# Optimization experiments

Measured on AMD Instinct MI355X. Metric: run time of the kernel, lower is better.

## Reference

```python
import jax, jax.numpy as jnp
import numpy as np


def setup_inputs() -> dict:
    key = jax.random.key(0)
    k1, k2, k3, k4 = jax.random.split(key, 4)
    N, Ck, Cv, T, H, W = 8, 128, 512, 8, 30, 30
    return {
        "q_key": jax.random.normal(k1, (N, Ck, H, W), dtype=jnp.float32),
        "q_val": jax.random.normal(k2, (N, Cv, H, W), dtype=jnp.float32),
        "m_key": jax.random.normal(k3, (N, Ck, T, H, W), dtype=jnp.float32),
        "m_val": jax.random.normal(k4, (N, Cv, T, H, W), dtype=jnp.float32),
    }


def reference(q_key, q_val, m_key, m_val):
    N, Ck, H, W = q_key.shape
    _, Cv, T, Hm, Wm = m_val.shape
    qk = q_key.reshape(N, Ck, H * W)            # n c q
    mk = m_key.reshape(N, Ck, T * Hm * Wm)      # n c m
    # affinity [n, q, m], scaled by 1/sqrt(Ck)
    aff = jnp.einsum("ncq,ncm->nqm", qk, mk) * (Ck ** -0.5)
    # NOTE: softmax over the QUERY axis (axis=1), per the original module
    attn = jax.nn.softmax(aff, axis=1)
    mv = m_val.reshape(N, Cv, T * Hm * Wm)      # n c m
    mapped = jnp.einsum("nqm,ncm->ncq", attn, mv).reshape(N, Cv, Hm, Wm)
    return jnp.concatenate([q_val, mapped], axis=1)  # [N, 2*Cv, H, W]
```

## Files before the change

kernel.cpp:

```cpp
#include <hip/hip_runtime.h>
#include <stdint.h>

#define N_  8
#define CK  128
#define CV  512
#define HW  900
#define M_  7200
#define QK_SCALE 0.08838834764831845f

typedef __attribute__((ext_vector_type(8))) short  short8;
typedef __attribute__((ext_vector_type(4))) float  floatx4;
typedef __attribute__((ext_vector_type(4))) unsigned int   uintx4;
typedef __attribute__((ext_vector_type(4))) unsigned short ushortx4;

__device__ __forceinline__ uint16_t f32_to_bf16(float x) {
    union { float f; uint32_t u; } v; v.f = x;
    return (uint16_t)((v.u + 0x7FFFu + ((v.u >> 16) & 1u)) >> 16);
}

__device__ __forceinline__ void gload_lds16(const uint16_t* g, short* l) {
    __builtin_amdgcn_global_load_lds(
        (const __attribute__((address_space(1))) void*)g,
        (__attribute__((address_space(3))) void*)l,
        16, 0, 0);
}

#define WAITV(n) asm volatile("s_waitcnt vmcnt(" #n ")" ::: "memory")
#define BARRIER() do { __builtin_amdgcn_sched_barrier(0); \
                       __builtin_amdgcn_s_barrier(); \
                       __builtin_amdgcn_sched_barrier(0); } while (0)

__global__ void k_zero(float* __restrict__ p) {
    int i = blockIdx.x * 256 + threadIdx.x;
    if (i < N_ * M_) p[i] = 0.f;
}

__global__ __launch_bounds__(256) void k_copy_qval(const float* __restrict__ qv,
                                                   float* __restrict__ out) {
    unsigned i = blockIdx.x * 256 + threadIdx.x;
    unsigned e = i * 4u;
    unsigned n = e / (CV * HW);
    unsigned off = e - n * (CV * HW);
    *(floatx4*)&out[(size_t)n * (2 * CV * HW) + off] = *(const floatx4*)&qv[e];
}

__global__ __launch_bounds__(256) void k_trans(const float* __restrict__ in,
                                               uint16_t* __restrict__ outp, int L) {
    __shared__ float tile[32][33];
    const int tx = threadIdx.x & 31;
    const int ty = threadIdx.x >> 5;
    const int l0 = blockIdx.x * 32;
    const int c0 = blockIdx.y * 32;
    const int n  = blockIdx.z;
    const float* src = in + (size_t)n * CK * L;
    uint16_t* dst = outp + (size_t)n * L * CK;
#pragma unroll
    for (int p = 0; p < 4; p++) {
        int c = c0 + p * 8 + ty;
        int l = l0 + tx;
        float v = 0.f;
        if (l < L) v = src[(size_t)c * L + l];
        tile[p * 8 + ty][tx] = v;
    }
    __syncthreads();
#pragma unroll
    for (int p = 0; p < 4; p++) {
        int l = l0 + p * 8 + ty;
        int c = c0 + tx;
        if (l < L) dst[(size_t)l * CK + c] = f32_to_bf16(tile[tx][p * 8 + ty]);
    }
}

#define K1_TS 144

__global__ __launch_bounds__(256) void k1_gemm_exp(
    const uint16_t* __restrict__ qkT,
    const uint16_t* __restrict__ mkT,
    uint16_t* __restrict__ E,
    float* __restrict__ dsum)
{
    __shared__ __align__(16) short smem[32768];
    __shared__ float colsum[128];

    const int bid = blockIdx.x + 57 * (blockIdx.y + 8 * blockIdx.z);
    const int swz = (bid & 7) * 456 + (bid >> 3);
    const int mb   = swz % 57;
    const int rest = swz / 57;
    const int m0 = mb * 128;
    const int q0 = (rest & 7) * 128;
    const int n  = rest >> 3;
    const int tid = threadIdx.x;

    if (tid < 128) colsum[tid] = 0.f;

    const int lane = tid & 63;
    const int wid  = tid >> 6;
    const int wq   = (wid >> 1) << 6;
    const int wm   = (wid & 1) << 6;
    const int fr   = lane & 15;
    const int quad = lane >> 4;

    const int ca = wid * 2;
    const int rr = lane >> 2;
    const int cc = (lane & 3) * 8;

    const uint16_t* Ab = qkT + (size_t)n * HW * CK;
    const uint16_t* Bb = mkT + (size_t)n * M_ * CK;
    const uint16_t* A0p = Ab + (size_t)(q0 + ca * 16 + rr) * CK + cc;
    const uint16_t* A1p = A0p + 16 * CK;
    const uint16_t* B0p = Bb + (size_t)(m0 + ca * 16 + rr) * CK + cc;
    const uint16_t* B1p = B0p + 16 * CK;

    floatx4 acc[4][4];
#pragma unroll
    for (int a = 0; a < 4; a++)
#pragma unroll
        for (int b = 0; b < 4; b++) acc[a][b] = (floatx4){0.f, 0.f, 0.f, 0.f};

#define K1_STAGE(buf, ko) do { \
    short* dA = smem + (buf) * 8192 + ca * 512; \
    short* dB = dA + 4096; \
    gload_lds16(A0p + (ko), dA); \
    gload_lds16(A1p + (ko), dA + 512); \
    gload_lds16(B0p + (ko), dB); \
    gload_lds16(B1p + (ko), dB + 512); \
} while (0)

#define K1_COMPUTE(buf) do { \
    const short* bA = smem + (buf) * 8192; \
    const short* bB = bA + 4096; \
    const int k0 = quad * 8; \
    short8 af[4], bfr[4]; \
    _Pragma("unroll") \
    for (int t = 0; t < 4; t++) \
        af[t] = *(const short8*)&bA[(wq + t * 16 + fr) * 32 + k0]; \
    _Pragma("unroll") \
    for (int t = 0; t < 4; t++) \
        bfr[t] = *(const short8*)&bB[(wm + t * 16 + fr) * 32 + k0]; \
    _Pragma("unroll") \
    for (int tq = 0; tq < 4; tq++) \
        _Pragma("unroll") \
        for (int tm = 0; tm < 4; tm++) \
            acc[tq][tm] = __builtin_amdgcn_mfma_f32_16x16x32_bf16( \
                af[tq], bfr[tm], acc[tq][tm], 0, 0, 0); \
} while (0)

    K1_STAGE(0, 0); K1_STAGE(1, 32); K1_STAGE(2, 64);
    WAITV(8); BARRIER(); K1_STAGE(3, 96); K1_COMPUTE(0);
    WAITV(8); BARRIER(); K1_COMPUTE(1);
    WAITV(4); BARRIER(); K1_COMPUTE(2);
    WAITV(0); BARRIER(); K1_COMPUTE(3);

    __syncthreads();
    float cs[4] = {0.f, 0.f, 0.f, 0.f};
#pragma unroll
    for (int tq = 0; tq < 4; tq++) {
#pragma unroll
        for (int tm = 0; tm < 4; tm++) {
            const int col = wm + tm * 16 + fr;
#pragma unroll
            for (int i = 0; i < 4; i++) {
                const int row = wq + tq * 16 + quad * 4 + i;
                float e = __expf(acc[tq][tm][i] * QK_SCALE);
                if (q0 + row < HW) cs[tm] += e;
                smem[row * K1_TS + col] = (short)f32_to_bf16(e);
            }
        }
    }
#pragma unroll
    for (int tm = 0; tm < 4; tm++) {
        float s = cs[tm];
        s += __shfl_xor(s, 16, 64);
        s += __shfl_xor(s, 32, 64);
        if (quad == 0) atomicAdd(&colsum[wm + tm * 16 + fr], s);
    }
    __syncthreads();

    uint16_t* En = E + (size_t)n * HW * M_;
#pragma unroll
    for (int j = 0; j < 8; j++) {
        int idx = tid + j * 256;
        int r   = idx >> 4;
        int c8  = (idx & 15) * 8;
        if (q0 + r < HW && m0 + c8 + 8 <= M_) {
            uintx4 v = *(const uintx4*)&smem[r * K1_TS + c8];
            *(uintx4*)&En[(size_t)(q0 + r) * M_ + m0 + c8] = v;
        }
    }
    if (tid < 128) {
        const int gm = m0 + tid;
        if (gm < M_) atomicAdd(&dsum[(size_t)n * M_ + gm], colsum[tid]);
    }
#undef K1_STAGE
#undef K1_COMPUTE
}

__global__ void k_dinv(const float* __restrict__ d, float* __restrict__ di) {
    int i = blockIdx.x * 256 + threadIdx.x;
    if (i < N_ * M_) di[i] = 1.0f / d[i];
}

__global__ __launch_bounds__(256) void k_mvs(
    const float* __restrict__ mval,
    const float* __restrict__ dinv,
    uint16_t* __restrict__ mvs)
{
    unsigned i = blockIdx.x * 256 + threadIdx.x;
    unsigned base = i * 4u;
    unsigned n = base / (unsigned)(CV * M_);
    unsigned m = base % (unsigned)M_;
    floatx4 v  = *(const floatx4*)&mval[base];
    floatx4 di = *(const floatx4*)&dinv[n * (unsigned)M_ + m];
    ushortx4 o;
    o[0] = f32_to_bf16(v[0] * di[0]);
    o[1] = f32_to_bf16(v[1] * di[1]);
    o[2] = f32_to_bf16(v[2] * di[2]);
    o[3] = f32_to_bf16(v[3] * di[3]);
    *(ushortx4*)&mvs[base] = o;
}

#define K2_SPLITS 3
#define K2_BK 32
#define K2_STEPS 75

__global__ __launch_bounds__(256) void k2_split3(
    const uint16_t* __restrict__ mvs,
    const uint16_t* __restrict__ E,
    float* __restrict__ partials)
{
    __shared__ __align__(16) short lds2[32768];

    const int bid = blockIdx.x + 8 * (blockIdx.y + 4 * blockIdx.z);
    const int swz = (bid & 7) * 96 + (bid >> 3);
    const int q0 = (swz & 7) << 7;
    const int c0 = ((swz >> 3) & 3) << 7;
    const int nz = swz >> 5;
    const int n     = nz / K2_SPLITS;
    const int split = nz - n * K2_SPLITS;
    const int tid = threadIdx.x;

    const int lane = tid & 63;
    const int wid  = tid >> 6;
    const int wc   = (wid >> 1) << 6;
    const int wq   = (wid & 1) << 6;
    const int fr   = lane & 15;
    const int quad = lane >> 4;

    const int ca = wid * 2;
    const int rr = lane >> 2;
    const int cc = (lane & 3) * 8;

    const uint16_t* Asrc = mvs + (size_t)(n * CV + c0) * M_ + split * 2400;
    const uint16_t* Bsrc = E + (size_t)n * HW * M_ + split * 2400;
    const uint16_t* A0p = Asrc + (size_t)(ca * 16 + rr) * M_ + cc;
    const uint16_t* A1p = A0p + (size_t)16 * M_;
    const uint16_t* B0p = Bsrc + (size_t)(q0 + ca * 16 + rr) * M_ + cc;
    const uint16_t* B1p = B0p + (size_t)16 * M_;

    floatx4 acc[4][4];
#pragma unroll
    for (int a = 0; a < 4; a++)
#pragma unroll
        for (int b = 0; b < 4; b++) acc[a][b] = (floatx4){0.f, 0.f, 0.f, 0.f};

#define K2_STAGE(buf, mo) do { \
    short* dA = lds2 + (buf) * 8192 + ca * 512; \
    short* dB = dA + 4096; \
    gload_lds16(A0p + (mo), dA); \
    gload_lds16(A1p + (mo), dA + 512); \
    gload_lds16(B0p + (mo), dB); \
    gload_lds16(B1p + (mo), dB + 512); \
} while (0)

#define K2_COMPUTE(buf) do { \
    const short* bA = lds2 + (buf) * 8192; \
    const short* bB = bA + 4096; \
    const int k0 = quad * 8; \
    short8 af[4], bfr[4]; \
    _Pragma("unroll") \
    for (int t = 0; t < 4; t++) \
        af[t] = *(const short8*)&bA[(wc + t * 16 + fr) * 32 + k0]; \
    _Pragma("unroll") \
    for (int t = 0; t < 4; t++) \
        bfr[t] = *(const short8*)&bB[(wq + t * 16 + fr) * 32 + k0]; \
    _Pragma("unroll") \
    for (int tc = 0; tc < 4; tc++) \
        _Pragma("unroll") \
        for (int tq = 0; tq < 4; tq++) \
            acc[tc][tq] = __builtin_amdgcn_mfma_f32_16x16x32_bf16( \
                af[tc], bfr[tq], acc[tc][tq], 0, 0, 0); \
} while (0)

    K2_STAGE(0, 0);
    K2_STAGE(1, K2_BK);
    K2_STAGE(2, 2 * K2_BK);
    for (int t = 0; t < K2_STEPS - 3; ++t) {
        WAITV(8); BARRIER();
        K2_STAGE((t + 3) & 3, (t + 3) * K2_BK);
        K2_COMPUTE(t & 3);
    }
    WAITV(8); BARRIER(); K2_COMPUTE(0);
    WAITV(4); BARRIER(); K2_COMPUTE(1);
    WAITV(0); BARRIER(); K2_COMPUTE(2);

    float* P = partials + ((size_t)split * N_ + n) * CV * HW;
#pragma unroll
    for (int tc = 0; tc < 4; tc++) {
#pragma unroll
        for (int tq = 0; tq < 4; tq++) {
            const int gq = q0 + wq + tq * 16 + fr;
            if (gq < HW) {
#pragma unroll
                for (int i = 0; i < 4; i++) {
                    const int gc = c0 + wc + tc * 16 + quad * 4 + i;
                    P[(size_t)gc * HW + gq] = acc[tc][tq][i];
                }
            }
        }
    }
#undef K2_STAGE
#undef K2_COMPUTE
}

__global__ __launch_bounds__(256) void k_reduce3(const float* __restrict__ partials,
                                                 float* __restrict__ out) {
    unsigned i = blockIdx.x * 256 + threadIdx.x;
    unsigned e = i * 4u;
    unsigned n = e / (CV * HW);
    unsigned off = e - n * (CV * HW);
    const size_t stride = (size_t)N_ * CV * HW;
    const float* p = partials + (size_t)n * CV * HW + off;
    floatx4 a = *(const floatx4*)&p[0];
    floatx4 b = *(const floatx4*)&p[stride];
    floatx4 c = *(const floatx4*)&p[2 * stride];
    floatx4 s = a + b + c;
    *(floatx4*)&out[(size_t)n * (2 * CV * HW) + CV * HW + off] = s;
}

extern "C" void kernel_launch(void* const* d_in, const int* in_sizes, int n_in,
                              void* d_out, int out_size, void* d_ws, size_t ws_size,
                              hipStream_t stream) {
    const float* qkey = (const float*)d_in[0];
    const float* qval = (const float*)d_in[1];
    const float* mkey = (const float*)d_in[2];
    const float* mval = (const float*)d_in[3];
    float* out = (float*)d_out;

    char* ws = (char*)d_ws;
    uint16_t* E        = (uint16_t*)ws;
    float*    dsum     = (float*)(ws + 103680000);
    float*    dinv     = (float*)(ws + 103910400);
    uint16_t* mvs      = (uint16_t*)(ws + 104140800);
    float*    partials = (float*)(ws + 163123200);
    uint16_t* qkT      = (uint16_t*)(ws + 163123200);
    uint16_t* mkT      = (uint16_t*)(ws + 163123200 + 1843200);

    (void)in_sizes; (void)n_in; (void)out_size; (void)ws_size;

    k_zero<<<dim3((N_ * M_ + 255) / 256), 256, 0, stream>>>(dsum);
    k_copy_qval<<<dim3((N_ * CV * HW) / 4 / 256), 256, 0, stream>>>(qval, out);
    k_trans<<<dim3(29, 4, N_), 256, 0, stream>>>(qkey, qkT, HW);
    k_trans<<<dim3(225, 4, N_), 256, 0, stream>>>(mkey, mkT, M_);
    k1_gemm_exp<<<dim3(57, 8, N_), 256, 0, stream>>>(qkT, mkT, E, dsum);
    k_dinv<<<dim3((N_ * M_ + 255) / 256), 256, 0, stream>>>(dsum, dinv);
    k_mvs<<<dim3((N_ * CV * M_) / 4 / 256), 256, 0, stream>>>(mval, dinv, mvs);
    k2_split3<<<dim3(8, 4, N_ * K2_SPLITS), 256, 0, stream>>>(mvs, E, partials);
    k_reduce3<<<dim3((N_ * CV * HW) / 4 / 256), 256, 0, stream>>>(partials, out);
}
```

Baseline: 414.8 us.

## Remove split-K in second GEMM, load E directly to registers, fuse reciprocal

Drops the three-way split-K and the reduction kernel, so the second GEMM writes final output directly. The E operand is loaded straight from global memory into registers with a 3-stage rotating buffer, while only mvs is staged in LDS. The reciprocal of the column sums is folded into the mvs scaling kernel, removing a launch. This removes the partials traffic and two launches, but cuts the grid to 256 blocks with long K loops and uses less coalesced direct global loads.

```diff
diff --git a/kernel.cpp b/kernel.cpp
--- a/kernel.cpp
+++ b/kernel.cpp
@@ -195,50 +195,41 @@
 #undef K1_COMPUTE
 }
 
-__global__ void k_dinv(const float* __restrict__ d, float* __restrict__ di) {
-    int i = blockIdx.x * 256 + threadIdx.x;
-    if (i < N_ * M_) di[i] = 1.0f / d[i];
-}
-
 __global__ __launch_bounds__(256) void k_mvs(
     const float* __restrict__ mval,
-    const float* __restrict__ dinv,
+    const float* __restrict__ dsum,
     uint16_t* __restrict__ mvs)
 {
     unsigned i = blockIdx.x * 256 + threadIdx.x;
     unsigned base = i * 4u;
     unsigned n = base / (unsigned)(CV * M_);
     unsigned m = base % (unsigned)M_;
-    floatx4 v  = *(const floatx4*)&mval[base];
-    floatx4 di = *(const floatx4*)&dinv[n * (unsigned)M_ + m];
+    floatx4 v = *(const floatx4*)&mval[base];
+    floatx4 d = *(const floatx4*)&dsum[n * (unsigned)M_ + m];
     ushortx4 o;
-    o[0] = f32_to_bf16(v[0] * di[0]);
-    o[1] = f32_to_bf16(v[1] * di[1]);
-    o[2] = f32_to_bf16(v[2] * di[2]);
-    o[3] = f32_to_bf16(v[3] * di[3]);
+    o[0] = f32_to_bf16(v[0] * (1.0f / d[0]));
+    o[1] = f32_to_bf16(v[1] * (1.0f / d[1]));
+    o[2] = f32_to_bf16(v[2] * (1.0f / d[2]));
+    o[3] = f32_to_bf16(v[3] * (1.0f / d[3]));
     *(ushortx4*)&mvs[base] = o;
 }
 
-#define K2_SPLITS 3
-#define K2_BK 32
-#define K2_STEPS 75
-
-__global__ __launch_bounds__(256) void k2_split3(
+#define K2_NT 225
+
+__global__ __launch_bounds__(256) void k2_direct(
     const uint16_t* __restrict__ mvs,
     const uint16_t* __restrict__ E,
-    float* __restrict__ partials)
+    float* __restrict__ out)
 {
-    __shared__ __align__(16) short lds2[32768];
+    __shared__ __align__(16) short ldsA[3 * 4096];
 
     const int bid = blockIdx.x + 8 * (blockIdx.y + 4 * blockIdx.z);
-    const int swz = (bid & 7) * 96 + (bid >> 3);
+    const int swz = (bid & 7) * 32 + (bid >> 3);
     const int q0 = (swz & 7) << 7;
     const int c0 = ((swz >> 3) & 3) << 7;
-    const int nz = swz >> 5;
-    const int n     = nz / K2_SPLITS;
-    const int split = nz - n * K2_SPLITS;
-    const int tid = threadIdx.x;
-
+    const int n  = swz >> 5;
+
+    const int tid  = threadIdx.x;
     const int lane = tid & 63;
     const int wid  = tid >> 6;
     const int wc   = (wid >> 1) << 6;
@@ -249,13 +240,14 @@
     const int ca = wid * 2;
     const int rr = lane >> 2;
     const int cc = (lane & 3) * 8;
-
-    const uint16_t* Asrc = mvs + (size_t)(n * CV + c0) * M_ + split * 2400;
-    const uint16_t* Bsrc = E + (size_t)n * HW * M_ + split * 2400;
-    const uint16_t* A0p = Asrc + (size_t)(ca * 16 + rr) * M_ + cc;
+    const uint16_t* A0p = mvs + (size_t)(n * CV + c0 + ca * 16 + rr) * M_ + cc;
     const uint16_t* A1p = A0p + (size_t)16 * M_;
-    const uint16_t* B0p = Bsrc + (size_t)(q0 + ca * 16 + rr) * M_ + cc;
-    const uint16_t* B1p = B0p + (size_t)16 * M_;
+
+    const uint16_t* En = E + (size_t)n * HW * M_;
+    const uint16_t* Bp0 = En + (size_t)(q0 + wq +  0 + fr) * M_ + quad * 8;
+    const uint16_t* Bp1 = En + (size_t)(q0 + wq + 16 + fr) * M_ + quad * 8;
+    const uint16_t* Bp2 = En + (size_t)(q0 + wq + 32 + fr) * M_ + quad * 8;
+    const uint16_t* Bp3 = En + (size_t)(q0 + wq + 48 + fr) * M_ + quad * 8;
 
     floatx4 acc[4][4];
 #pragma unroll
@@ -263,47 +255,60 @@
 #pragma unroll
         for (int b = 0; b < 4; b++) acc[a][b] = (floatx4){0.f, 0.f, 0.f, 0.f};
 
-#define K2_STAGE(buf, mo) do { \
-    short* dA = lds2 + (buf) * 8192 + ca * 512; \
-    short* dB = dA + 4096; \
-    gload_lds16(A0p + (mo), dA); \
-    gload_lds16(A1p + (mo), dA + 512); \
-    gload_lds16(B0p + (mo), dB); \
-    gload_lds16(B1p + (mo), dB + 512); \
-} while (0)
-
-#define K2_COMPUTE(buf) do { \
-    const short* bA = lds2 + (buf) * 8192; \
-    const short* bB = bA + 4096; \
-    const int k0 = quad * 8; \
-    short8 af[4], bfr[4]; \
+    short8 breg[3][4];
+
+#define K2_STAGE_A(buf, mo) do { \
+    gload_lds16(A0p + (mo), ldsA + (buf) * 4096 + ca * 512); \
+    gload_lds16(A1p + (mo), ldsA + (buf) * 4096 + ca * 512 + 512); \
+} while (0)
+
+#define K2_LOAD_B(r, mo) do { \
+    breg[r][0] = *(const short8*)(Bp0 + (mo)); \
+    breg[r][1] = *(const short8*)(Bp1 + (mo)); \
+    breg[r][2] = *(const short8*)(Bp2 + (mo)); \
+    breg[r][3] = *(const short8*)(Bp3 + (mo)); \
+} while (0)
+
+#define K2_COMPUTE(bA, rC) do { \
+    const short* pA = ldsA + (bA) * 4096; \
+    short8 af[4]; \
     _Pragma("unroll") \
     for (int t = 0; t < 4; t++) \
-        af[t] = *(const short8*)&bA[(wc + t * 16 + fr) * 32 + k0]; \
-    _Pragma("unroll") \
-    for (int t = 0; t < 4; t++) \
-        bfr[t] = *(const short8*)&bB[(wq + t * 16 + fr) * 32 + k0]; \
+        af[t] = *(const short8*)&pA[(wc + t * 16 + fr) * 32 + quad * 8]; \
     _Pragma("unroll") \
     for (int tc = 0; tc < 4; tc++) \
         _Pragma("unroll") \
         for (int tq = 0; tq < 4; tq++) \
             acc[tc][tq] = __builtin_amdgcn_mfma_f32_16x16x32_bf16( \
-                af[tc], bfr[tq], acc[tc][tq], 0, 0, 0); \
-} while (0)
-
-    K2_STAGE(0, 0);
-    K2_STAGE(1, K2_BK);
-    K2_STAGE(2, 2 * K2_BK);
-    for (int t = 0; t < K2_STEPS - 3; ++t) {
-        WAITV(8); BARRIER();
-        K2_STAGE((t + 3) & 3, (t + 3) * K2_BK);
-        K2_COMPUTE(t & 3);
-    }
-    WAITV(8); BARRIER(); K2_COMPUTE(0);
-    WAITV(4); BARRIER(); K2_COMPUTE(1);
-    WAITV(0); BARRIER(); K2_COMPUTE(2);
-
-    float* P = partials + ((size_t)split * N_ + n) * CV * HW;
+                af[tc], breg[rC][tq], acc[tc][tq], 0, 0, 0); \
+} while (0)
+
+    K2_STAGE_A(0, 0);
+    K2_LOAD_B(0, 0);
+    K2_STAGE_A(1, 32);
+
+    int ao = 64;
+    int bo = 32;
+    for (int s = 0; s < 74; s++) {
+        WAITV(6); BARRIER();
+        K2_STAGE_A(2, ao); K2_LOAD_B(1, bo); K2_COMPUTE(0, 0);
+        ao += 32; bo += 32;
+        WAITV(6); BARRIER();
+        K2_STAGE_A(0, ao); K2_LOAD_B(2, bo); K2_COMPUTE(1, 1);
+        ao += 32; bo += 32;
+        WAITV(6); BARRIER();
+        K2_STAGE_A(1, ao); K2_LOAD_B(0, bo); K2_COMPUTE(2, 2);
+        ao += 32; bo += 32;
+    }
+    WAITV(6); BARRIER();
+    K2_STAGE_A(2, ao); K2_LOAD_B(1, bo); K2_COMPUTE(0, 0);
+    bo += 32;
+    WAITV(6); BARRIER();
+    K2_LOAD_B(2, bo); K2_COMPUTE(1, 1);
+    WAITV(4); BARRIER();
+    K2_COMPUTE(2, 2);
+
+    float* On = out + (size_t)n * (2 * CV * HW) + (size_t)CV * HW;
 #pragma unroll
     for (int tc = 0; tc < 4; tc++) {
 #pragma unroll
@@ -313,28 +318,14 @@
 #pragma unroll
                 for (int i = 0; i < 4; i++) {
                     const int gc = c0 + wc + tc * 16 + quad * 4 + i;
-                    P[(size_t)gc * HW + gq] = acc[tc][tq][i];
+                    On[(size_t)gc * HW + gq] = acc[tc][tq][i];
                 }
             }
         }
     }
-#undef K2_STAGE
+#undef K2_STAGE_A
+#undef K2_LOAD_B
 #undef K2_COMPUTE
-}
-
-__global__ __launch_bounds__(256) void k_reduce3(const float* __restrict__ partials,
-                                                 float* __restrict__ out) {
-    unsigned i = blockIdx.x * 256 + threadIdx.x;
-    unsigned e = i * 4u;
-    unsigned n = e / (CV * HW);
-    unsigned off = e - n * (CV * HW);
-    const size_t stride = (size_t)N_ * CV * HW;
-    const float* p = partials + (size_t)n * CV * HW + off;
-    floatx4 a = *(const floatx4*)&p[0];
-    floatx4 b = *(const floatx4*)&p[stride];
-    floatx4 c = *(const floatx4*)&p[2 * stride];
-    floatx4 s = a + b + c;
-    *(floatx4*)&out[(size_t)n * (2 * CV * HW) + CV * HW + off] = s;
 }
 
 extern "C" void kernel_launch(void* const* d_in, const int* in_sizes, int n_in,
@@ -349,9 +340,7 @@
     char* ws = (char*)d_ws;
     uint16_t* E        = (uint16_t*)ws;
     float*    dsum     = (float*)(ws + 103680000);
-    float*    dinv     = (float*)(ws + 103910400);
     uint16_t* mvs      = (uint16_t*)(ws + 104140800);
-    float*    partials = (float*)(ws + 163123200);
     uint16_t* qkT      = (uint16_t*)(ws + 163123200);
     uint16_t* mkT      = (uint16_t*)(ws + 163123200 + 1843200);
 
@@ -362,8 +351,6 @@
     k_trans<<<dim3(29, 4, N_), 256, 0, stream>>>(qkey, qkT, HW);
     k_trans<<<dim3(225, 4, N_), 256, 0, stream>>>(mkey, mkT, M_);
     k1_gemm_exp<<<dim3(57, 8, N_), 256, 0, stream>>>(qkT, mkT, E, dsum);
-    k_dinv<<<dim3((N_ * M_ + 255) / 256), 256, 0, stream>>>(dsum, dinv);
-    k_mvs<<<dim3((N_ * CV * M_) / 4 / 256), 256, 0, stream>>>(mval, dinv, mvs);
-    k2_split3<<<dim3(8, 4, N_ * K2_SPLITS), 256, 0, stream>>>(mvs, E, partials);
-    k_reduce3<<<dim3((N_ * CV * HW) / 4 / 256), 256, 0, stream>>>(partials, out);
-}
+    k_mvs<<<dim3((N_ * CV * M_) / 4 / 256), 256, 0, stream>>>(mval, dsum, mvs);
+    k2_direct<<<dim3(8, 4, 8), 256, 0, stream>>>(mvs, E, out);
+}
```

Measured after the change: 489.6 us. +18.0%, slower.
